# Optimization experiments

Hardware: AMD Instinct MI355X
Metric: run time of the kernel (lower is better)

## Reference

```python
import jax, jax.numpy as jnp
import numpy as np

PARTIAL_DATA_THRESHOLD = 0.1  # threshold on squared NN distance (ChamferDistance returns squared dists)


def setup_inputs() -> dict:
    key = jax.random.key(0)
    k1, k2 = jax.random.split(key)
    scan_vertices = jax.random.normal(k1, (50000, 3), dtype=jnp.float32)      # N x 3
    template_vertices = jax.random.normal(k2, (6890, 3), dtype=jnp.float32)   # M x 3
    return {"scan_vertices": scan_vertices, "template_vertices": template_vertices}


def reference(scan_vertices, template_vertices):
    # Directional (template -> scan) Chamfer: for each template point, squared
    # distance to nearest scan point; then sum distances below threshold.
    # d2[m, n] = |t_m|^2 + |s_n|^2 - 2 t_m . s_n
    t_sq = jnp.sum(template_vertices * template_vertices, axis=-1)            # [M]
    s_sq = jnp.sum(scan_vertices * scan_vertices, axis=-1)                    # [N]
    cross = jnp.einsum('md,nd->mn', template_vertices, scan_vertices)         # [M, N]
    d2 = t_sq[:, None] + s_sq[None, :] - 2.0 * cross                          # [M, N]
    template2scan = jnp.min(d2, axis=1)                                       # [M]
    mask = template2scan < PARTIAL_DATA_THRESHOLD
    return jnp.sum(jnp.where(mask, template2scan, 0.0))
```

## Files before the change

### kernel.cpp

```cpp
#include <hip/hip_runtime.h>
#include <hip/hip_bf16.h>

#define TM 9
#define BLK 256
#define TPB (BLK * TM)
#define SCPAD 152
#define THRESH 0.1f
#define KEY_MAX 0xFFFFFFFFu

__device__ __forceinline__ unsigned int f2key(float f) {
    unsigned int b = __float_as_uint(f);
    return (b & 0x80000000u) ? ~b : (b | 0x80000000u);
}
__device__ __forceinline__ float key2f(unsigned int k) {
    return __uint_as_float((k & 0x80000000u) ? (k & 0x7FFFFFFFu) : ~k);
}

__global__ __launch_bounds__(BLK) void pdl_init(unsigned int* __restrict__ gmin,
                                                float* __restrict__ out, int Mpad) {
    const int i = blockIdx.x * BLK + threadIdx.x;
    if (i < Mpad) gmin[i] = KEY_MAX;
    if (i == 0) out[0] = 0.0f;
}

__global__ __launch_bounds__(BLK) void pdl_main(const float* __restrict__ scan,
                                                const float* __restrict__ tmpl,
                                                unsigned int* __restrict__ gmin,
                                                int M, int N) {
    __shared__ float4 sp[SCPAD];
    const int tid = threadIdx.x;

    const int j0 = blockIdx.x * SCPAD;
    for (int p = tid; p < SCPAD; p += BLK) {
        const int j = j0 + p;
        float4 q = make_float4(0.0f, 0.0f, 0.0f, 3e30f);
        if (j < N) {
            const float x = scan[3 * j + 0];
            const float y = scan[3 * j + 1];
            const float z = scan[3 * j + 2];
            q = make_float4(-2.0f * x, -2.0f * y, -2.0f * z, x * x + y * y + z * z);
        }
        sp[p] = q;
    }

    const int m0 = blockIdx.y * TPB + tid;
    float tx[TM], ty[TM], tz[TM], t2[TM], mn[TM];
#pragma unroll
    for (int k = 0; k < TM; ++k) {
        int m = m0 + k * BLK;
        if (m >= M) m = M - 1;
        const float x = tmpl[3 * m + 0];
        const float y = tmpl[3 * m + 1];
        const float z = tmpl[3 * m + 2];
        tx[k] = x; ty[k] = y; tz[k] = z;
        t2[k] = x * x + y * y + z * z;
        mn[k] = 3e30f;
    }

    __syncthreads();

#pragma unroll 2
    for (int jj = 0; jj < SCPAD; jj += 4) {
        const float4 s0 = sp[jj + 0];
        const float4 s1 = sp[jj + 1];
        const float4 s2 = sp[jj + 2];
        const float4 s3 = sp[jj + 3];
#pragma unroll
        for (int k = 0; k < TM; ++k) {
            const float e0 = fmaf(s0.x, tx[k], fmaf(s0.y, ty[k], fmaf(s0.z, tz[k], s0.w)));
            const float e1 = fmaf(s1.x, tx[k], fmaf(s1.y, ty[k], fmaf(s1.z, tz[k], s1.w)));
            const float e2 = fmaf(s2.x, tx[k], fmaf(s2.y, ty[k], fmaf(s2.z, tz[k], s2.w)));
            const float e3 = fmaf(s3.x, tx[k], fmaf(s3.y, ty[k], fmaf(s3.z, tz[k], s3.w)));
            const float x = fminf(fminf(e0, e1), e2);
            mn[k] = fminf(fminf(x, e3), mn[k]);
        }
    }

#pragma unroll
    for (int k = 0; k < TM; ++k) {
        const int m = m0 + k * BLK;
        if (m < M) atomicMin(&gmin[m], f2key(mn[k] + t2[k]));
    }
}

__global__ __launch_bounds__(BLK) void pdl_final(const unsigned int* __restrict__ gmin,
                                                 float* __restrict__ out, int M) {
    const int m = blockIdx.x * BLK + threadIdx.x;
    float s = 0.0f;
    if (m < M) {
        const float v = key2f(gmin[m]);
        if (v < THRESH) s = v;
    }

#pragma unroll
    for (int off = 32; off > 0; off >>= 1) s += __shfl_down(s, off, 64);

    __shared__ float ls[BLK / 64];
    const int lane = threadIdx.x & 63;
    const int w = threadIdx.x >> 6;
    if (lane == 0) ls[w] = s;
    __syncthreads();
    if (threadIdx.x == 0) {
        float t = 0.0f;
#pragma unroll
        for (int i = 0; i < BLK / 64; ++i) t += ls[i];
        atomicAdd(out, t);
    }
}

extern "C" void kernel_launch(void* const* d_in, const int* in_sizes, int n_in,
                              void* d_out, int out_size, void* d_ws, size_t ws_size,
                              hipStream_t stream) {
    const float* scan = (const float*)d_in[0];
    const float* tmpl = (const float*)d_in[1];
    float* out = (float*)d_out;

    const int N = in_sizes[0] / 3;
    const int M = in_sizes[1] / 3;

    const int sChunks = (N + SCPAD - 1) / SCPAD;
    const int tChunks = (M + TPB - 1) / TPB;
    const int Mpad = tChunks * TPB;

    unsigned int* gmin = (unsigned int*)d_ws;

    pdl_init<<<(Mpad + BLK - 1) / BLK, BLK, 0, stream>>>(gmin, out, Mpad);

    dim3 grid(sChunks, tChunks);
    pdl_main<<<grid, BLK, 0, stream>>>(scan, tmpl, gmin, M, N);

    pdl_final<<<(M + BLK - 1) / BLK, BLK, 0, stream>>>(gmin, out, M);
}
```

Measured before the change: 87.07 us.

## Compute pairwise distances with bf16x2-split MFMA instead of scalar FMA

```diff
diff --git a/kernel.cpp b/kernel.cpp
--- a/kernel.cpp
+++ b/kernel.cpp
@@ -1,89 +1,154 @@
 #include <hip/hip_runtime.h>
 #include <hip/hip_bf16.h>
 
-#define TM 9
 #define BLK 256
-#define TPB (BLK * TM)
-#define SCPAD 152
+#define SCPAD 1024
+#define FRAGS (SCPAD / 32)
 #define THRESH 0.1f
 #define KEY_MAX 0xFFFFFFFFu
-
-__device__ __forceinline__ unsigned int f2key(float f) {
-    unsigned int b = __float_as_uint(f);
+#define ONE_BF ((unsigned short)0x3F80)
+
+typedef __attribute__((ext_vector_type(8))) short short8;
+typedef __attribute__((ext_vector_type(16))) float floatx16;
+
+__device__ __forceinline__ unsigned short f2bf(float x) {
+    unsigned u = __float_as_uint(x);
+    unsigned r = u + 0x7FFFu + ((u >> 16) & 1u);
+    return (unsigned short)(r >> 16);
+}
+__device__ __forceinline__ float bf2f(unsigned short h) {
+    return __uint_as_float(((unsigned)h) << 16);
+}
+
+__device__ __forceinline__ unsigned f2key(float f) {
+    unsigned b = __float_as_uint(f);
     return (b & 0x80000000u) ? ~b : (b | 0x80000000u);
 }
-__device__ __forceinline__ float key2f(unsigned int k) {
+__device__ __forceinline__ float key2f(unsigned k) {
     return __uint_as_float((k & 0x80000000u) ? (k & 0x7FFFFFFFu) : ~k);
 }
 
-__global__ __launch_bounds__(BLK) void pdl_init(unsigned int* __restrict__ gmin,
-                                                float* __restrict__ out, int Mpad) {
-    const int i = blockIdx.x * BLK + threadIdx.x;
-    if (i < Mpad) gmin[i] = KEY_MAX;
-    if (i == 0) out[0] = 0.0f;
-}
-
-__global__ __launch_bounds__(BLK) void pdl_main(const float* __restrict__ scan,
-                                                const float* __restrict__ tmpl,
-                                                unsigned int* __restrict__ gmin,
-                                                int M, int N) {
-    __shared__ float4 sp[SCPAD];
+__global__ __launch_bounds__(BLK) void pdl_prep(const float* __restrict__ scan,
+                                                uint4* __restrict__ fragbuf,
+                                                unsigned* __restrict__ gmin,
+                                                float* __restrict__ out,
+                                                int N, int NSLOT, int Mpad) {
+    const int n = blockIdx.x * BLK + threadIdx.x;
+    if (n == 0) out[0] = 0.0f;
+    if (n < Mpad) gmin[n] = KEY_MAX;
+    if (n >= NSLOT) return;
+
+    unsigned short k[16];
+    if (n < N) {
+        const float x = scan[3 * n + 0], y = scan[3 * n + 1], z = scan[3 * n + 2];
+        const float s2 = fmaf(x, x, fmaf(y, y, z * z));
+        const float cx = -2.0f * x, cy = -2.0f * y, cz = -2.0f * z;
+        const unsigned short xh = f2bf(cx); const unsigned short xl = f2bf(cx - bf2f(xh));
+        const unsigned short yh = f2bf(cy); const unsigned short yl = f2bf(cy - bf2f(yh));
+        const unsigned short zh = f2bf(cz); const unsigned short zl = f2bf(cz - bf2f(zh));
+        const unsigned short wh = f2bf(s2); const unsigned short wl = f2bf(s2 - bf2f(wh));
+        k[0] = xh; k[1] = xl; k[2] = xh; k[3] = xl;
+        k[4] = yh; k[5] = yl; k[6] = yh; k[7] = yl;
+        k[8] = zh; k[9] = zl; k[10] = zh; k[11] = zl;
+        k[12] = ONE_BF; k[13] = ONE_BF;
+        k[14] = wh; k[15] = wl;
+    } else {
+#pragma unroll
+        for (int i = 0; i < 16; ++i) k[i] = 0;
+        k[12] = ONE_BF; k[13] = ONE_BF;
+        k[14] = f2bf(1e30f); k[15] = 0;
+    }
+
+    const int g = n >> 5, c = n & 31;
+    uint4 lo, hi;
+    lo.x = (unsigned)k[0] | ((unsigned)k[1] << 16);
+    lo.y = (unsigned)k[2] | ((unsigned)k[3] << 16);
+    lo.z = (unsigned)k[4] | ((unsigned)k[5] << 16);
+    lo.w = (unsigned)k[6] | ((unsigned)k[7] << 16);
+    hi.x = (unsigned)k[8] | ((unsigned)k[9] << 16);
+    hi.y = (unsigned)k[10] | ((unsigned)k[11] << 16);
+    hi.z = (unsigned)k[12] | ((unsigned)k[13] << 16);
+    hi.w = (unsigned)k[14] | ((unsigned)k[15] << 16);
+    fragbuf[(size_t)g * 64 + c] = lo;
+    fragbuf[(size_t)g * 64 + 32 + c] = hi;
+}
+
+__global__ __launch_bounds__(BLK) void pdl_main(const float* __restrict__ tmpl,
+                                                const uint4* __restrict__ fragbuf,
+                                                unsigned* __restrict__ gmin, int M) {
+    __shared__ uint4 sm[FRAGS * 64];
     const int tid = threadIdx.x;
-
-    const int j0 = blockIdx.x * SCPAD;
-    for (int p = tid; p < SCPAD; p += BLK) {
-        const int j = j0 + p;
-        float4 q = make_float4(0.0f, 0.0f, 0.0f, 3e30f);
-        if (j < N) {
-            const float x = scan[3 * j + 0];
-            const float y = scan[3 * j + 1];
-            const float z = scan[3 * j + 2];
-            q = make_float4(-2.0f * x, -2.0f * y, -2.0f * z, x * x + y * y + z * z);
+    const int wave = tid >> 6, lane = tid & 63;
+
+    const uint4* src = fragbuf + (size_t)blockIdx.x * (FRAGS * 64);
+    for (int i = tid; i < FRAGS * 64; i += BLK) sm[i] = src[i];
+
+    const int tbase = blockIdx.y * 256 + wave * 64;
+    short8 A[2];
+#pragma unroll
+    for (int af = 0; af < 2; ++af) {
+        int m = tbase + af * 32 + (lane & 31);
+        if (m > M - 1) m = M - 1;
+        const float x = tmpl[3 * m + 0], y = tmpl[3 * m + 1], z = tmpl[3 * m + 2];
+        const float t2 = fmaf(x, x, fmaf(y, y, z * z));
+        const unsigned short xh = f2bf(x); const unsigned short xl = f2bf(x - bf2f(xh));
+        const unsigned short yh = f2bf(y); const unsigned short yl = f2bf(y - bf2f(yh));
+        const unsigned short zh = f2bf(z); const unsigned short zl = f2bf(z - bf2f(zh));
+        const unsigned short wh = f2bf(t2); const unsigned short wl = f2bf(t2 - bf2f(wh));
+        const bool hi = (lane >= 32);
+        short8 a;
+        a[0] = (short)(hi ? zh : xh);
+        a[1] = (short)(hi ? zh : xh);
+        a[2] = (short)(hi ? zl : xl);
+        a[3] = (short)(hi ? zl : xl);
+        a[4] = (short)(hi ? wh : yh);
+        a[5] = (short)(hi ? wl : yh);
+        a[6] = (short)(hi ? ONE_BF : yl);
+        a[7] = (short)(hi ? ONE_BF : yl);
+        A[af] = a;
+    }
+
+    float mn0[16], mn1[16];
+#pragma unroll
+    for (int r = 0; r < 16; ++r) { mn0[r] = 3e30f; mn1[r] = 3e30f; }
+
+    __syncthreads();
+
+    union U { uint4 u; short8 s; };
+    for (int f = 0; f < FRAGS; ++f) {
+        U t; t.u = sm[f * 64 + lane];
+        const short8 B = t.s;
+        floatx16 acc0, acc1;
+#pragma unroll
+        for (int r = 0; r < 16; ++r) { acc0[r] = 0.0f; acc1[r] = 0.0f; }
+        acc0 = __builtin_amdgcn_mfma_f32_32x32x16_bf16(A[0], B, acc0, 0, 0, 0);
+        acc1 = __builtin_amdgcn_mfma_f32_32x32x16_bf16(A[1], B, acc1, 0, 0, 0);
+#pragma unroll
+        for (int r = 0; r < 16; ++r) {
+            mn0[r] = fminf(mn0[r], acc0[r]);
+            mn1[r] = fminf(mn1[r], acc1[r]);
         }
-        sp[p] = q;
-    }
-
-    const int m0 = blockIdx.y * TPB + tid;
-    float tx[TM], ty[TM], tz[TM], t2[TM], mn[TM];
-#pragma unroll
-    for (int k = 0; k < TM; ++k) {
-        int m = m0 + k * BLK;
-        if (m >= M) m = M - 1;
-        const float x = tmpl[3 * m + 0];
-        const float y = tmpl[3 * m + 1];
-        const float z = tmpl[3 * m + 2];
-        tx[k] = x; ty[k] = y; tz[k] = z;
-        t2[k] = x * x + y * y + z * z;
-        mn[k] = 3e30f;
-    }
-
-    __syncthreads();
-
-#pragma unroll 2
-    for (int jj = 0; jj < SCPAD; jj += 4) {
-        const float4 s0 = sp[jj + 0];
-        const float4 s1 = sp[jj + 1];
-        const float4 s2 = sp[jj + 2];
-        const float4 s3 = sp[jj + 3];
-#pragma unroll
-        for (int k = 0; k < TM; ++k) {
-            const float e0 = fmaf(s0.x, tx[k], fmaf(s0.y, ty[k], fmaf(s0.z, tz[k], s0.w)));
-            const float e1 = fmaf(s1.x, tx[k], fmaf(s1.y, ty[k], fmaf(s1.z, tz[k], s1.w)));
-            const float e2 = fmaf(s2.x, tx[k], fmaf(s2.y, ty[k], fmaf(s2.z, tz[k], s2.w)));
-            const float e3 = fmaf(s3.x, tx[k], fmaf(s3.y, ty[k], fmaf(s3.z, tz[k], s3.w)));
-            const float x = fminf(fminf(e0, e1), e2);
-            mn[k] = fminf(fminf(x, e3), mn[k]);
+    }
+
+#pragma unroll
+    for (int af = 0; af < 2; ++af) {
+#pragma unroll
+        for (int r = 0; r < 16; ++r) {
+            float v = (af == 0) ? mn0[r] : mn1[r];
+            v = fminf(v, __shfl_xor(v, 1, 32));
+            v = fminf(v, __shfl_xor(v, 2, 32));
+            v = fminf(v, __shfl_xor(v, 4, 32));
+            v = fminf(v, __shfl_xor(v, 8, 32));
+            v = fminf(v, __shfl_xor(v, 16, 32));
+            if ((lane & 31) == 0) {
+                const int row = (r & 3) + 8 * (r >> 2) + ((lane >> 5) << 2);
+                atomicMin(&gmin[tbase + af * 32 + row], f2key(v));
+            }
         }
     }
-
-#pragma unroll
-    for (int k = 0; k < TM; ++k) {
-        const int m = m0 + k * BLK;
-        if (m < M) atomicMin(&gmin[m], f2key(mn[k] + t2[k]));
-    }
-}
-
-__global__ __launch_bounds__(BLK) void pdl_final(const unsigned int* __restrict__ gmin,
+}
+
+__global__ __launch_bounds__(BLK) void pdl_final(const unsigned* __restrict__ gmin,
                                                  float* __restrict__ out, int M) {
     const int m = blockIdx.x * BLK + threadIdx.x;
     float s = 0.0f;
@@ -91,7 +156,6 @@
         const float v = key2f(gmin[m]);
         if (v < THRESH) s = v;
     }
-
 #pragma unroll
     for (int off = 32; off > 0; off >>= 1) s += __shfl_down(s, off, 64);
 
@@ -119,15 +183,19 @@
     const int M = in_sizes[1] / 3;
 
     const int sChunks = (N + SCPAD - 1) / SCPAD;
-    const int tChunks = (M + TPB - 1) / TPB;
-    const int Mpad = tChunks * TPB;
-
-    unsigned int* gmin = (unsigned int*)d_ws;
-
-    pdl_init<<<(Mpad + BLK - 1) / BLK, BLK, 0, stream>>>(gmin, out, Mpad);
-
-    dim3 grid(sChunks, tChunks);
-    pdl_main<<<grid, BLK, 0, stream>>>(scan, tmpl, gmin, M, N);
+    const int NSLOT = sChunks * SCPAD;
+    const int tGroups = (M + 255) / 256;
+    const int Mpad = tGroups * 256;
+
+    unsigned* gmin = (unsigned*)d_ws;
+    uint4* fragbuf = (uint4*)((char*)d_ws + 65536);
+
+    const int prepThreads = (NSLOT > Mpad ? NSLOT : Mpad);
+    pdl_prep<<<(prepThreads + BLK - 1) / BLK, BLK, 0, stream>>>(scan, fragbuf, gmin,
+                                                               out, N, NSLOT, Mpad);
+
+    dim3 grid(sChunks, tGroups);
+    pdl_main<<<grid, BLK, 0, stream>>>(tmpl, fragbuf, gmin, M);
 
     pdl_final<<<(M + BLK - 1) / BLK, BLK, 0, stream>>>(gmin, out, M);
 }
```

Result: slower. 97.45 us (+11.9%).
